# Performance work log

Measured on AMD Instinct MI355X. Metric: run time of the kernel, lower is better.

Reference implementation:

```python
import jax, jax.numpy as jnp
import numpy as np
from jax import lax

P_LEN, Q_LEN, B = 400, 60, 128
P_IN, Q_IN, H = 512, 512, 256
D = P_IN + Q_IN  # gate / GRU input size


def setup_inputs() -> dict:
    key = jax.random.key(0)
    ks = jax.random.split(key, 10)
    s = 0.05  # small init scale to keep tanh/sigmoid in sane range
    return {
        "q_input": jax.random.normal(ks[0], (Q_LEN, B, Q_IN), jnp.float32),
        "p_input": jax.random.normal(ks[1], (P_LEN, B, P_IN), jnp.float32),
        "q_mask": jnp.zeros((Q_LEN, B), dtype=bool),
        "Wq": jax.random.normal(ks[2], (2, Q_IN, H), jnp.float32) * s,
        "Wp": jax.random.normal(ks[3], (2, P_IN, H), jnp.float32) * s,
        "Ws": jax.random.normal(ks[4], (2, H, H), jnp.float32) * s,
        "v": jax.random.normal(ks[5], (2, H, 1), jnp.float32) * s,
        "gate_W": jax.random.normal(ks[6], (2, D, D), jnp.float32) * s,
        "gate_b": jnp.zeros((2, D), jnp.float32),
        "gru_Wih": jax.random.normal(ks[7], (2, 3 * H, D), jnp.float32) * s,
        "gru_Whh": jax.random.normal(ks[8], (2, 3 * H, H), jnp.float32) * s,
        "gru_bih": jnp.zeros((2, 3 * H), jnp.float32),
        "gru_bhh": jnp.zeros((2, 3 * H), jnp.float32),
    }


def _run_direction(q_input, p_input, q_mask, Wq, Wp, Ws, v,
                   gate_W, gate_b, gru_Wih, gru_Whh, gru_bih, gru_bhh,
                   reverse):
    # q_input: [Q, B, q_in], p_input: [P, B, p_in], q_mask: [Q, B] bool
    hid = Ws.shape[1]
    q_temp = jnp.einsum('qbe,eh->qbh', q_input, Wq)  # precomputed once, [Q,B,H]
    p_temp = jnp.einsum('pbe,eh->pbh', p_input, Wp)  # [P,B,H]
    mask = q_mask[:, :, None]                        # [Q,B,1]

    def step(state, xs):
        p_x, p_t = xs  # [B,p_in], [B,H]
        state_temp = state @ Ws                                   # [B,H]
        logits = jnp.tanh(q_temp + p_t[None] + state_temp[None]) @ v  # [Q,B,1]
        logits = jnp.where(mask, -jnp.inf, logits)
        weights = jax.nn.softmax(logits, axis=0)                  # over q_len
        att = jnp.sum(weights * q_input, axis=0)                  # [B,q_in]
        x = jnp.concatenate([p_x, att], axis=-1)                  # [B,D]
        x = x * jax.nn.sigmoid(x @ gate_W.T + gate_b)             # Gate
        # torch GRUCell math
        gi = x @ gru_Wih.T + gru_bih
        gh = state @ gru_Whh.T + gru_bhh
        i_r, i_z, i_n = jnp.split(gi, 3, axis=-1)
        h_r, h_z, h_n = jnp.split(gh, 3, axis=-1)
        r = jax.nn.sigmoid(i_r + h_r)
        z = jax.nn.sigmoid(i_z + h_z)
        n = jnp.tanh(i_n + r * h_n)
        new_state = (1.0 - z) * n + z * state
        return new_state, new_state

    init = jnp.zeros((p_input.shape[1], hid), p_input.dtype)
    _, out = lax.scan(step, init, (p_input, p_temp), reverse=reverse)
    return out  # [P,B,H], already in original time order (scan reverse handles it)


def reference(q_input, p_input, q_mask, Wq, Wp, Ws, v, gate_W, gate_b,
              gru_Wih, gru_Whh, gru_bih, gru_bhh):
    out_fw = _run_direction(q_input, p_input, q_mask, Wq[0], Wp[0], Ws[0], v[0],
                            gate_W[0], gate_b[0], gru_Wih[0], gru_Whh[0],
                            gru_bih[0], gru_bhh[0], reverse=False)
    out_bw = _run_direction(q_input, p_input, q_mask, Wq[1], Wp[1], Ws[1], v[1],
                            gate_W[1], gate_b[1], gru_Wih[1], gru_Whh[1],
                            gru_bih[1], gru_bhh[1], reverse=True)
    return jnp.concatenate([out_fw, out_bw], axis=-1)  # [P,B,2H]
```

## Files before the change

### kernel.cpp

```cpp
#include <hip/hip_runtime.h>

#define PL 400
#define QL 60
#define BB 128
#define EE 512
#define HH 256
#define DD 1024
#define G3 768
#define NBLK 256
#define NTHR 512
#define LDK 72

typedef __attribute__((ext_vector_type(8))) short bfrag;
typedef __attribute__((ext_vector_type(4))) float facc;
typedef __attribute__((ext_vector_type(4))) unsigned uintx4;

__device__ __forceinline__ unsigned short f2bf(float x) {
  unsigned u = __float_as_uint(x);
  return (unsigned short)((u + 0x7fffu + ((u >> 16) & 1u)) >> 16);
}
__device__ __forceinline__ float bf2f(unsigned short h) {
  return __uint_as_float(((unsigned)h) << 16);
}
__device__ __forceinline__ void split_bf(float x, unsigned short& hi, unsigned short& lo) {
  hi = f2bf(x);
  lo = f2bf(x - bf2f(hi));
}
__device__ __forceinline__ unsigned packf(float x) {
  unsigned short hi, lo;
  split_bf(x, hi, lo);
  return ((unsigned)hi << 16) | lo;
}
__device__ __forceinline__ float unpk(unsigned p) {
  return bf2f((unsigned short)(p >> 16)) + bf2f((unsigned short)(p & 0xffffu));
}
__device__ __forceinline__ float sigm(float x) {
  return __builtin_amdgcn_rcpf(1.f + __expf(-x));
}
__device__ __forceinline__ float ftanh(float x) {
  float xc = fminf(fmaxf(x, -10.f), 10.f);
  float t = __expf(2.f * xc);
  return (t - 1.f) * __builtin_amdgcn_rcpf(t + 1.f);
}

__device__ __forceinline__ float ald(const float* p) {
  return __hip_atomic_load((float*)p, __ATOMIC_RELAXED, __HIP_MEMORY_SCOPE_AGENT);
}
__device__ __forceinline__ void ast(float* p, float v) {
  __hip_atomic_store(p, v, __ATOMIC_RELAXED, __HIP_MEMORY_SCOPE_AGENT);
}
__device__ __forceinline__ unsigned aldu(const unsigned* p) {
  return __hip_atomic_load((unsigned*)p, __ATOMIC_RELAXED, __HIP_MEMORY_SCOPE_AGENT);
}
__device__ __forceinline__ void astu(unsigned* p, unsigned v) {
  __hip_atomic_store(p, v, __ATOMIC_RELAXED, __HIP_MEMORY_SCOPE_AGENT);
}
__device__ __forceinline__ unsigned long long aldull(const unsigned long long* p) {
  return __hip_atomic_load((unsigned long long*)p, __ATOMIC_RELAXED, __HIP_MEMORY_SCOPE_AGENT);
}
__device__ __forceinline__ void pollge(unsigned* f, unsigned tgt) {
  unsigned sp = 0;
  while (aldu(f) < tgt) {
    __builtin_amdgcn_s_sleep(1);
    if (++sp > (1u << 26)) break;
  }
}

constexpr size_t SZ_QT  = (size_t)2 * QL * BB * HH;
constexpr size_t SZ_PT  = (size_t)2 * PL * BB * HH;
constexpr size_t SZ_GIP = (size_t)2 * 4 * BB * G3;
constexpr size_t SZ_GHP = (size_t)2 * BB * G3;
constexpr size_t SZ_WST = (size_t)2 * HH * HH;
constexpr size_t OFF_QT  = 0;
constexpr size_t OFF_PT  = OFF_QT + SZ_QT;
constexpr size_t OFF_GIP = OFF_PT + SZ_PT;
constexpr size_t OFF_GHP = OFF_GIP + SZ_GIP;
constexpr size_t OFF_WST = OFF_GHP + SZ_GHP;
constexpr size_t F32_TOT = OFF_WST + SZ_WST;
constexpr size_t UOFF_ATTP  = 0;
constexpr size_t UOFF_XPACK = UOFF_ATTP + (size_t)2 * 2 * BB * EE;
constexpr size_t UOFF_HPACK = UOFF_XPACK + (size_t)2 * 2 * BB * DD;
constexpr size_t U_TOT      = UOFF_HPACK + (size_t)2 * BB * HH;
constexpr size_t HSZ_WQT = (size_t)2 * HH * EE;
constexpr size_t HSZ_GW  = (size_t)2 * DD * DD;
constexpr size_t HSZ_WIH = (size_t)2 * G3 * DD;
constexpr size_t HSZ_WHH = (size_t)2 * G3 * HH;
constexpr size_t HOFF_WQTH = 0;
constexpr size_t HOFF_WQTL = HOFF_WQTH + HSZ_WQT;
constexpr size_t HOFF_WPTH = HOFF_WQTL + HSZ_WQT;
constexpr size_t HOFF_WPTL = HOFF_WPTH + HSZ_WQT;
constexpr size_t HOFF_GWH  = HOFF_WPTL + HSZ_WQT;
constexpr size_t HOFF_GWL  = HOFF_GWH + HSZ_GW;
constexpr size_t HOFF_WIHH = HOFF_GWL + HSZ_GW;
constexpr size_t HOFF_WIHL = HOFF_WIHH + HSZ_WIH;
constexpr size_t HOFF_WHHH = HOFF_WIHL + HSZ_WIH;
constexpr size_t HOFF_WHHL = HOFF_WHHH + HSZ_WHH;
constexpr size_t HOFF_QIN16 = HOFF_WHHL + HSZ_WHH;
constexpr size_t H_TOT      = HOFF_QIN16 + (size_t)QL * BB * EE;

#define FA 0
#define FG 256
#define FI 320
#define FH 416
#define FC 440

__device__ __forceinline__ void gbar(unsigned* slots, unsigned gen) {
  asm volatile("" ::: "memory");
  __syncthreads();
  if (threadIdx.x == 0)
    __hip_atomic_store(&slots[blockIdx.x], gen, __ATOMIC_RELAXED, __HIP_MEMORY_SCOPE_AGENT);
  if (threadIdx.x < NBLK) pollge(&slots[threadIdx.x], gen);
  __syncthreads();
  asm volatile("" ::: "memory");
}

template <int NT, bool BSPLIT, int NCH, int ASRC>
__device__ void gemm_direct(facc* acc,
                            const unsigned short* wh, const unsigned short* wl,
                            const unsigned* apk, const float* a32, int as,
                            int kbase, int wchbase) {
  const int tid = threadIdx.x;
  const int lane = tid & 63;
  const int w = tid >> 6;
  constexpr int FN = NT / 16;
  const int lr = lane & 15;
  const int lk = (lane >> 4) << 3;
  const int row = (w << 4) + lr;

#pragma unroll 2
  for (int ch = 0; ch < NCH; ++ch) {
    const int kk = kbase + (ch << 6);
#pragma unroll
    for (int k32 = 0; k32 < 64; k32 += 32) {
      const int ko = kk + k32 + lk;
      bfrag ah, al_;
      {
        unsigned hu[4], lu[4];
        if constexpr (ASRC == 0) {
          const unsigned long long* src =
              (const unsigned long long*)(apk + (size_t)row * as + ko);
          unsigned long long d0 = aldull(src + 0);
          unsigned long long d1 = aldull(src + 1);
          unsigned long long d2 = aldull(src + 2);
          unsigned long long d3 = aldull(src + 3);
          unsigned p0 = (unsigned)d0, p1 = (unsigned)(d0 >> 32);
          unsigned p2 = (unsigned)d1, p3 = (unsigned)(d1 >> 32);
          unsigned p4 = (unsigned)d2, p5 = (unsigned)(d2 >> 32);
          unsigned p6 = (unsigned)d3, p7 = (unsigned)(d3 >> 32);
          hu[0] = (p0 >> 16) | (p1 & 0xffff0000u);  lu[0] = (p0 & 0xffffu) | (p1 << 16);
          hu[1] = (p2 >> 16) | (p3 & 0xffff0000u);  lu[1] = (p2 & 0xffffu) | (p3 << 16);
          hu[2] = (p4 >> 16) | (p5 & 0xffff0000u);  lu[2] = (p4 & 0xffffu) | (p5 << 16);
          hu[3] = (p6 >> 16) | (p7 & 0xffff0000u);  lu[3] = (p6 & 0xffffu) | (p7 << 16);
        } else {
          const float* src = a32 + (size_t)row * as + ko;
          float4 v0 = *(const float4*)src;
          float4 v1 = *(const float4*)(src + 4);
          unsigned short h0, l0, h1, l1;
          split_bf(v0.x, h0, l0); split_bf(v0.y, h1, l1);
          hu[0] = h0 | ((unsigned)h1 << 16); lu[0] = l0 | ((unsigned)l1 << 16);
          split_bf(v0.z, h0, l0); split_bf(v0.w, h1, l1);
          hu[1] = h0 | ((unsigned)h1 << 16); lu[1] = l0 | ((unsigned)l1 << 16);
          split_bf(v1.x, h0, l0); split_bf(v1.y, h1, l1);
          hu[2] = h0 | ((unsigned)h1 << 16); lu[2] = l0 | ((unsigned)l1 << 16);
          split_bf(v1.z, h0, l0); split_bf(v1.w, h1, l1);
          hu[3] = h0 | ((unsigned)h1 << 16); lu[3] = l0 | ((unsigned)l1 << 16);
        }
        uintx4 hv = {hu[0], hu[1], hu[2], hu[3]};
        uintx4 lv = {lu[0], lu[1], lu[2], lu[3]};
        ah  = __builtin_bit_cast(bfrag, hv);
        al_ = __builtin_bit_cast(bfrag, lv);
      }
      bfrag bhf[FN], blf[FN];
#pragma unroll
      for (int f = 0; f < FN; f++) {
        const int bo = ((wchbase + ch) * NT + (f << 4) + lr) * LDK + k32 + lk;
        bhf[f] = *(const bfrag*)&wh[bo];
        if constexpr (BSPLIT) blf[f] = *(const bfrag*)&wl[bo];
      }
#pragma unroll
      for (int j = 0; j < FN; j++) {
        acc[j] = __builtin_amdgcn_mfma_f32_16x16x32_bf16(al_, bhf[j], acc[j], 0, 0, 0);
        if constexpr (BSPLIT)
          acc[j] = __builtin_amdgcn_mfma_f32_16x16x32_bf16(ah, blf[j], acc[j], 0, 0, 0);
        acc[j] = __builtin_amdgcn_mfma_f32_16x16x32_bf16(ah, bhf[j], acc[j], 0, 0, 0);
      }
    }
  }
}

__device__ void gemm_pro(unsigned short* sAh, unsigned short* sAl, unsigned short* warea,
                         const float* a32,
                         const unsigned short* bh_g, const unsigned short* bl_g,
                         float* dst) {
  const int tid = threadIdx.x;
  const int lane = tid & 63;
  const int w = tid >> 6;
  const int wm = (w >> 2) << 6;
  const int wn = (w & 3) << 5;
  const int lr = lane & 15;
  const int lk = (lane >> 4) << 3;
  unsigned short* wh = warea;
  unsigned short* wl = warea + 128 * LDK;
  const facc fz = {0.f, 0.f, 0.f, 0.f};
  facc acc[4][2];
#pragma unroll
  for (int i = 0; i < 4; i++)
#pragma unroll
    for (int j = 0; j < 2; j++) acc[i][j] = fz;
  for (int ch = 0; ch < 8; ++ch) {
    const int kk0 = ch << 6;
    for (int i = tid; i < 8192; i += NTHR) {
      const int r = i >> 6, k = i & 63;
      unsigned short uh, ul;
      split_bf(a32[(size_t)r * EE + kk0 + k], uh, ul);
      sAh[r * LDK + k] = uh;
      sAl[r * LDK + k] = ul;
      wh[r * LDK + k] = bh_g[(size_t)r * EE + kk0 + k];
      wl[r * LDK + k] = bl_g[(size_t)r * EE + kk0 + k];
    }
    __syncthreads();
#pragma unroll
    for (int k32 = 0; k32 < 64; k32 += 32) {
      bfrag ah[4], al_[4], bhf[2], blf[2];
#pragma unroll
      for (int f = 0; f < 4; f++) {
        const int ao = (wm + (f << 4) + lr) * LDK + k32 + lk;
        ah[f]  = *(const bfrag*)&sAh[ao];
        al_[f] = *(const bfrag*)&sAl[ao];
      }
#pragma unroll
      for (int f = 0; f < 2; f++) {
        const int bo = (wn + (f << 4) + lr) * LDK + k32 + lk;
        bhf[f] = *(const bfrag*)&wh[bo];
        blf[f] = *(const bfrag*)&wl[bo];
      }
#pragma unroll
      for (int i = 0; i < 4; i++)
#pragma unroll
        for (int j = 0; j < 2; j++) {
          acc[i][j] = __builtin_amdgcn_mfma_f32_16x16x32_bf16(al_[i], bhf[j], acc[i][j], 0, 0, 0);
          acc[i][j] = __builtin_amdgcn_mfma_f32_16x16x32_bf16(ah[i], blf[j], acc[i][j], 0, 0, 0);
          acc[i][j] = __builtin_amdgcn_mfma_f32_16x16x32_bf16(ah[i], bhf[j], acc[i][j], 0, 0, 0);
        }
    }
    __syncthreads();
  }
  const int orow = (lane >> 4) << 2;
  const int ocol = lane & 15;
#pragma unroll
  for (int i = 0; i < 4; i++)
#pragma unroll
    for (int j = 0; j < 2; j++)
#pragma unroll
      for (int q = 0; q < 4; q++)
        dst[(size_t)(wm + (i << 4) + orow + q) * HH + (wn + (j << 4) + ocol)] = acc[i][j][q];
}

__global__ void __launch_bounds__(256) k_transpose_qp(
    const float* __restrict__ Wq, const float* __restrict__ Wp,
    unsigned short* __restrict__ wqth, unsigned short* __restrict__ wqtl,
    unsigned short* __restrict__ wpth, unsigned short* __restrict__ wptl) {
  __shared__ float tile[64 * 65];
  const int blk = blockIdx.x;
  const int mat = blk >> 6;
  const int rem = blk & 63;
  const int d = rem >> 5;
  const int rem2 = rem & 31;
  const int kt = rem2 >> 2;
  const int nt = rem2 & 3;
  const float* src = mat ? Wp : Wq;
  unsigned short* dh = mat ? wpth : wqth;
  unsigned short* dl = mat ? wptl : wqtl;
  const int tid = threadIdx.x;
  for (int i = tid; i < 4096; i += 256) {
    int kr = i >> 6, nc = i & 63;
    tile[kr * 65 + nc] = src[((size_t)d * EE + kt * 64 + kr) * HH + nt * 64 + nc];
  }
  __syncthreads();
  for (int i = tid; i < 4096; i += 256) {
    int n = i >> 6, k = i & 63;
    unsigned short hi, lo;
    split_bf(tile[k * 65 + n], hi, lo);
    size_t o = ((size_t)d * HH + nt * 64 + n) * EE + kt * 64 + k;
    dh[o] = hi; dl[o] = lo;
  }
}

__global__ void __launch_bounds__(256) k_split_w(
    const float* __restrict__ gw, const float* __restrict__ wih, const float* __restrict__ whh,
    unsigned short* __restrict__ gwh, unsigned short* __restrict__ gwl,
    unsigned short* __restrict__ wihh, unsigned short* __restrict__ wihl,
    unsigned short* __restrict__ whhh, unsigned short* __restrict__ whhl) {
  const size_t N1 = HSZ_GW, N2 = HSZ_WIH, N3 = HSZ_WHH;
  for (size_t i = (size_t)blockIdx.x * 256 + threadIdx.x; i < N1 + N2 + N3;
       i += (size_t)gridDim.x * 256) {
    float x; unsigned short *ph, *pl; size_t o;
    if (i < N1)           { o = i;           x = gw[o];  ph = gwh;  pl = gwl; }
    else if (i < N1 + N2) { o = i - N1;      x = wih[o]; ph = wihh; pl = wihl; }
    else                  { o = i - N1 - N2; x = whh[o]; ph = whhh; pl = whhl; }
    unsigned short hi, lo;
    split_bf(x, hi, lo);
    ph[o] = hi; pl[o] = lo;
  }
}

__global__ void __launch_bounds__(256) k_wst_qin(const float* __restrict__ Ws,
                                                 float* __restrict__ wst,
                                                 const float* __restrict__ qin,
                                                 unsigned short* __restrict__ qin16) {
  const size_t NQ = (size_t)QL * BB * EE;
  for (size_t i = (size_t)blockIdx.x * 256 + threadIdx.x; i < SZ_WST + NQ;
       i += (size_t)gridDim.x * 256) {
    if (i < SZ_WST) {
      int d = (int)(i >> 16);
      int j = (int)((i >> 8) & 255);
      int k = (int)(i & 255);
      wst[i] = Ws[((size_t)d * HH + k) * HH + j];
    } else {
      size_t o = i - SZ_WST;
      qin16[o] = f2bf(qin[o]);
    }
  }
}

__global__ void __launch_bounds__(NTHR, 1) pe_main(
    const float* __restrict__ qin, const float* __restrict__ pin,
    const unsigned char* __restrict__ qmask,
    const float* __restrict__ vvec, const float* __restrict__ gateb,
    const float* __restrict__ bih, const float* __restrict__ bhh,
    float* __restrict__ out,
    float* __restrict__ fws, unsigned* __restrict__ upck,
    unsigned short* __restrict__ hws, unsigned* __restrict__ bar) {
  __shared__ __align__(16) unsigned short smem[56320];
  unsigned short* sAh = smem;
  unsigned short* sAl = smem + 9216;
  unsigned short* warea = smem + 18432;
  float* fsm = (float*)smem;
  float* sv_perm   = (float*)(smem + 55296);
  float* sstv_perm = (float*)(smem + 55808);

  float* qt   = fws + OFF_QT;
  float* pt   = fws + OFF_PT;
  float* gip  = fws + OFF_GIP;
  float* ghp  = fws + OFF_GHP;
  float* wst  = fws + OFF_WST;
  unsigned* attp0 = upck + UOFF_ATTP;
  unsigned* xpck0 = upck + UOFF_XPACK;
  unsigned* hpack = upck + UOFF_HPACK;
  unsigned short* wqth = hws + HOFF_WQTH;
  unsigned short* wqtl = hws + HOFF_WQTL;
  unsigned short* wpth = hws + HOFF_WPTH;
  unsigned short* wptl = hws + HOFF_WPTL;
  unsigned short* gwh  = hws + HOFF_GWH;
  unsigned short* wihh = hws + HOFF_WIHH;
  unsigned short* wihl = hws + HOFF_WIHL;
  unsigned short* whhh = hws + HOFF_WHHH;
  unsigned short* whhl = hws + HOFF_WHHL;
  const unsigned short* qin16 = hws + HOFF_QIN16;
  unsigned* flg = bar + 256;

  const int blk = blockIdx.x;
  const int tid = threadIdx.x;
  const int lane = tid & 63;
  const int w = tid >> 6;

  const bool isGate = (blk < 64);
  const bool isGi   = (blk >= 64 && blk < 160);
  const bool isGh   = (blk >= 160 && blk < 184);
  const int gd = blk >> 5, gct = blk & 31, coloff = gct * 32;
  const int gi_g = blk - 64, id_ = gi_g / 48, ir = gi_g % 48;
  const int int_ = ir >> 2, iks = ir & 3;
  const int gh_g = blk - 160, hd = gh_g / 12, hnt = gh_g % 12;

  for (int tt = blk; tt < 1840; tt += NBLK) {
    if (tt < 1600) {
      int d = tt / 800, rem = tt % 800, mt = rem >> 1, ntp = rem & 1;
      gemm_pro(sAh, sAl, warea, pin + (size_t)mt * BB * EE,
               wpth + ((size_t)d * HH + ntp * 128) * EE,
               wptl + ((size_t)d * HH + ntp * 128) * EE,
               pt + ((size_t)d * PL * BB + (size_t)mt * BB) * HH + ntp * 128);
    } else {
      int u2 = tt - 1600;
      int d = u2 / 120, rem = u2 % 120, mt = rem >> 1, ntp = rem & 1;
      gemm_pro(sAh, sAl, warea, qin + (size_t)mt * BB * EE,
               wqth + ((size_t)d * HH + ntp * 128) * EE,
               wqtl + ((size_t)d * HH + ntp * 128) * EE,
               qt + ((size_t)d * QL * BB + (size_t)mt * BB) * HH + ntp * 128);
    }
  }

  if (isGate) {
    const unsigned short* src = gwh + (size_t)(gd * DD + coloff) * DD;
    for (int i = tid; i < 32768; i += NTHR) {
      int ch = i >> 11, n = (i >> 6) & 31, k = i & 63;
      warea[(ch * 32 + n) * LDK + k] = src[(size_t)n * DD + ch * 64 + k];
    }
  } else if (isGi) {
    const unsigned short* sh = wihh + (size_t)(id_ * G3 + int_ * 64) * DD + iks * 256;
    const unsigned short* sl = wihl + (size_t)(id_ * G3 + int_ * 64) * DD + iks * 256;
    for (int i = tid; i < 16384; i += NTHR) {
      int ch = i >> 12, n = (i >> 6) & 63, k = i & 63;
      warea[(ch * 64 + n) * LDK + k]         = sh[(size_t)n * DD + ch * 64 + k];
      warea[18432 + (ch * 64 + n) * LDK + k] = sl[(size_t)n * DD + ch * 64 + k];
    }
  } else if (isGh) {
    const unsigned short* sh = whhh + (size_t)(hd * G3 + hnt * 64) * HH;
    const unsigned short* sl = whhl + (size_t)(hd * G3 + hnt * 64) * HH;
    for (int i = tid; i < 16384; i += NTHR) {
      int ch = i >> 12, n = (i >> 6) & 63, k = i & 63;
      warea[(ch * 64 + n) * LDK + k]         = sh[(size_t)n * HH + ch * 64 + k];
      warea[18432 + (ch * 64 + n) * LDK + k] = sl[(size_t)n * HH + ch * 64 + k];
    }
  }

  __builtin_amdgcn_fence(__ATOMIC_RELEASE, "agent");
  gbar(bar, 1);

  const int d_ab = blk >> 7, b_ab = blk & 127;
  if (tid < 256) {
    sv_perm[tid] = vvec[d_ab * HH + tid];
    sstv_perm[tid] = 0.f;
  }
  const bool qmv = (tid < 64 && lane < QL) ? (qmask[lane * BB + b_ab] != 0) : false;
  __syncthreads();

  facc pinacc[2];
  if (isGate) {
    const facc fz = {0.f, 0.f, 0.f, 0.f};
    pinacc[0] = fz; pinacc[1] = fz;
    const int t0 = gd ? (PL - 1) : 0;
    gemm_direct<32, false, 8, 1>(pinacc, warea, nullptr,
                                 nullptr, pin + (size_t)t0 * BB * EE, EE, 0, 0);
  }

  float hreg = 0.f;
  float* sm = fsm;
  float* slog = fsm + 512;
  float* swgt = fsm + 576;
  float* spart = fsm + 896;
  float* hrow = fsm + 1408;

  for (int s = 0; s < PL; ++s) {
    const int par = s & 1;
    unsigned* attp = attp0 + (size_t)par * 2 * BB * EE;
    unsigned* xpack = xpck0 + (size_t)par * 2 * BB * DD;
    const unsigned gen = (unsigned)(s + 1);

    {
      const int d = d_ab, b = b_ab;
      const int t = d ? (PL - 1 - s) : s;
      if (tid < 256) {
        float ptv = __builtin_nontemporal_load(&pt[(((size_t)d * PL + t) * BB + b) * HH + tid]);
        sm[tid] = sstv_perm[tid] + ptv;
      }
      __syncthreads();
      for (int q = w; q < QL; q += 8) {
        float a = 0.f;
#pragma unroll
        for (int jj = 0; jj < 4; jj++) {
          int j = lane + jj * 64;
          a += ftanh(qt[(((size_t)d * QL + q) * BB + b) * HH + j] + sm[j]) * sv_perm[j];
        }
        for (int off = 32; off; off >>= 1) a += __shfl_down(a, off, 64);
        if (lane == 0) slog[q] = a;
      }
      __syncthreads();
      if (tid < 64) {
        float x = -3.0e38f;
        if (lane < QL) {
          x = slog[lane];
          if (qmv) x = -3.0e38f;
        }
        float mx = x;
        for (int off = 32; off; off >>= 1) mx = fmaxf(mx, __shfl_xor(mx, off, 64));
        float e = (lane < QL) ? __expf(x - mx) : 0.f;
        float sum2 = e;
        for (int off = 32; off; off >>= 1) sum2 += __shfl_xor(sum2, off, 64);
        if (lane < QL) swgt[lane] = e * __builtin_amdgcn_rcpf(sum2);
      }
      __syncthreads();
      {
        const int c = tid;
        float a0 = 0.f, a1 = 0.f, a2 = 0.f, a3 = 0.f;
        const unsigned short* qb = qin16 + (size_t)b * EE + c;
        for (int q = 0; q < QL; q += 4) {
          a0 += swgt[q]     * bf2f(qb[(size_t)q * BB * EE]);
          a1 += swgt[q + 1] * bf2f(qb[(size_t)(q + 1) * BB * EE]);
          a2 += swgt[q + 2] * bf2f(qb[(size_t)(q + 2) * BB * EE]);
          a3 += swgt[q + 3] * bf2f(qb[(size_t)(q + 3) * BB * EE]);
        }
        astu(&attp[((size_t)d * BB + b) * EE + c], packf((a0 + a1) + (a2 + a3)));
      }
      __syncthreads();
      if (tid == 0) astu(&flg[FA + d_ab * 128 + b_ab], gen);
    }

    const int orow = (lane >> 4) << 2;
    const int ocol = lane & 15;
    const int rbase = w << 4;

    if (isGate) {
      if (tid < 128) pollge(&flg[FA + gd * 128 + tid], gen);
      __syncthreads();
      gemm_direct<32, false, 8, 0>(pinacc, warea, nullptr,
                                   attp + (size_t)gd * BB * EE, nullptr, EE, 0, 8);
      {
        const int t = gd ? (PL - 1 - s) : s;
        const float* pin_t = pin + (size_t)t * BB * EE;
#pragma unroll
        for (int i = 0; i < 2; i++)
#pragma unroll
          for (int q = 0; q < 4; q++) {
            const int row = rbase + orow + q;
            const int gcol = coloff + (i << 4) + ocol;
            float uv = (gct < 16) ? pin_t[(size_t)row * EE + gcol]
                                  : unpk(aldu(&attp[((size_t)gd * BB + row) * EE + gcol - EE]));
            float x = uv * sigm(pinacc[i][q] + gateb[(size_t)gd * DD + gcol]);
            astu(&xpack[((size_t)gd * BB + row) * DD + gcol], packf(x));
          }
      }
      __syncthreads();
      if (tid == 0) astu(&flg[FG + gd * 32 + gct], gen);
      if (s + 1 < PL) {
        const facc fz = {0.f, 0.f, 0.f, 0.f};
        pinacc[0] = fz; pinacc[1] = fz;
        const int t2 = gd ? (PL - 2 - s) : (s + 1);
        gemm_direct<32, false, 8, 1>(pinacc, warea, nullptr,
                                     nullptr, pin + (size_t)t2 * BB * EE, EE, 0, 0);
      }
    } else if (isGi) {
      if (tid < 8) pollge(&flg[FG + id_ * 32 + iks * 8 + tid], gen);
      __syncthreads();
      const facc fz = {0.f, 0.f, 0.f, 0.f};
      facc acc[4] = {fz, fz, fz, fz};
      gemm_direct<64, true, 4, 0>(acc, warea, warea + 18432,
                                  xpack + (size_t)id_ * BB * DD, nullptr, DD, iks * 256, 0);
#pragma unroll
      for (int j = 0; j < 4; j++)
#pragma unroll
        for (int q = 0; q < 4; q++) {
          const int row = rbase + orow + q;
          const int col = int_ * 64 + (j << 4) + ocol;
          ast(&gip[((size_t)(id_ * 4 + iks) * BB + row) * G3 + col], acc[j][q]);
        }
      __syncthreads();
      if (tid == 0) astu(&flg[FI + id_ * 48 + ir], gen);
    } else if (isGh) {
      if (s > 0 && tid < 128) pollge(&flg[FC + hd * 128 + tid], (unsigned)s);
      __syncthreads();
      const facc fz = {0.f, 0.f, 0.f, 0.f};
      facc acc[4] = {fz, fz, fz, fz};
      gemm_direct<64, true, 4, 0>(acc, warea, warea + 18432,
                                  hpack + (size_t)hd * BB * HH, nullptr, HH, 0, 0);
#pragma unroll
      for (int j = 0; j < 4; j++)
#pragma unroll
        for (int q = 0; q < 4; q++) {
          const int row = rbase + orow + q;
          const int col = hnt * 64 + (j << 4) + ocol;
          ast(&ghp[((size_t)hd * BB + row) * G3 + col], acc[j][q]);
        }
      __syncthreads();
      if (tid == 0) astu(&flg[FH + hd * 12 + hnt], gen);
    }

    {
      if (tid < 48) pollge(&flg[FI + d_ab * 48 + tid], gen);
      else if (tid < 60) pollge(&flg[FH + d_ab * 12 + (tid - 48)], gen);
      __syncthreads();
      const int d = d_ab, b = b_ab;
      const int j = tid & 255, half = tid >> 8;
      const int t = d ? (PL - 1 - s) : s;
      const size_t rb = (size_t)d * BB + b;
      float gi3[3], gh3[3];
#pragma unroll
      for (int c3 = 0; c3 < 3; c3++) {
        float acc2 = bih[(size_t)d * G3 + c3 * HH + j];
#pragma unroll
        for (int ks = 0; ks < 4; ks++)
          acc2 += ald(&gip[((size_t)(d * 4 + ks) * BB + b) * G3 + c3 * HH + j]);
        gi3[c3] = acc2;
        gh3[c3] = ald(&ghp[rb * G3 + c3 * HH + j]) + bhh[(size_t)d * G3 + c3 * HH + j];
      }
      float r = sigm(gi3[0] + gh3[0]);
      float z = sigm(gi3[1] + gh3[1]);
      float n = ftanh(gi3[2] + r * gh3[2]);
      float hn = (1.f - z) * n + z * hreg;
      hreg = hn;
      if (half == 0) {
        __builtin_nontemporal_store(hn, &out[((size_t)t * BB + b) * 512 + d * HH + j]);
        astu(&hpack[rb * HH + j], packf(hn));
        hrow[j] = hn;
      }
      __syncthreads();
      if (tid == 0) astu(&flg[FC + d_ab * 128 + b_ab], gen);
      float part = 0.f;
      const float* wr = wst + ((size_t)d * HH + j) * HH + (half << 7);
      const float* hr = hrow + (half << 7);
#pragma unroll
      for (int k = 0; k < 128; k += 4) {
        float4 w4 = *(const float4*)&wr[k];
        float4 h4 = *(const float4*)&hr[k];
        part += w4.x * h4.x + w4.y * h4.y + w4.z * h4.z + w4.w * h4.w;
      }
      spart[tid] = part;
      __syncthreads();
      if (tid < 256) sstv_perm[tid] = spart[tid] + spart[tid + 256];
      __syncthreads();
    }
  }
}

extern "C" void kernel_launch(void* const* d_in, const int* in_sizes, int n_in,
                              void* d_out, int out_size, void* d_ws, size_t ws_size,
                              hipStream_t stream) {
  const float* qin = (const float*)d_in[0];
  const float* pin = (const float*)d_in[1];
  const unsigned char* qmask = (const unsigned char*)d_in[2];
  const float* Wq  = (const float*)d_in[3];
  const float* Wp  = (const float*)d_in[4];
  const float* Ws  = (const float*)d_in[5];
  const float* v   = (const float*)d_in[6];
  const float* gw  = (const float*)d_in[7];
  const float* gb  = (const float*)d_in[8];
  const float* wih = (const float*)d_in[9];
  const float* whh = (const float*)d_in[10];
  const float* bih = (const float*)d_in[11];
  const float* bhh = (const float*)d_in[12];
  float* out = (float*)d_out;

  char* base = (char*)d_ws;
  float* fws = (float*)base;
  unsigned* upck = (unsigned*)(base + F32_TOT * sizeof(float));
  unsigned short* hws = (unsigned short*)(base + F32_TOT * sizeof(float) + U_TOT * sizeof(unsigned));
  unsigned* bar = (unsigned*)(base + F32_TOT * sizeof(float) + U_TOT * sizeof(unsigned) +
                              H_TOT * sizeof(unsigned short));
  size_t need = F32_TOT * sizeof(float) + U_TOT * sizeof(unsigned) +
                H_TOT * sizeof(unsigned short) + 8192;
  if (ws_size < need) return;

  hipMemsetAsync(upck + UOFF_HPACK, 0, (size_t)2 * BB * HH * sizeof(unsigned), stream);
  hipMemsetAsync(bar, 0, 4096, stream);

  k_transpose_qp<<<128, 256, 0, stream>>>(Wq, Wp,
      hws + HOFF_WQTH, hws + HOFF_WQTL, hws + HOFF_WPTH, hws + HOFF_WPTL);
  k_split_w<<<1024, 256, 0, stream>>>(gw, wih, whh,
      hws + HOFF_GWH, hws + HOFF_GWL, hws + HOFF_WIHH, hws + HOFF_WIHL,
      hws + HOFF_WHHH, hws + HOFF_WHHL);
  k_wst_qin<<<2048, 256, 0, stream>>>(Ws, fws + OFF_WST, qin,
                                      hws + HOFF_QIN16);
  pe_main<<<NBLK, NTHR, 0, stream>>>(qin, pin, qmask, v, gb, bih, bhh, out,
                                     fws, upck, hws, bar);
}
```

Baseline: 20.54 ms.

## Move q/p projection GEMMs to separate kernel and add release fences on flags

The Wq/Wp projection GEMMs move out of the persistent pe_main loop into a standalone k_qtpt kernel launched with 1840 blocks. Kernel-launch ordering now replaces the grid-wide barrier that pe_main used to need before its recurrent phase. Each flag publish gets an agent-scope release fence, each poll gets a compiler scheduling fence, and the output store becomes a normal store instead of a nontemporal one. This lets the GEMM phase use full-device occupancy rather than 256 persistent blocks, at the cost of an extra launch and extra fence instructions on every recurrent step.

```diff
diff --git a/kernel.cpp b/kernel.cpp
--- a/kernel.cpp
+++ b/kernel.cpp
@@ -64,6 +64,10 @@
     __builtin_amdgcn_s_sleep(1);
     if (++sp > (1u << 26)) break;
   }
+}
+__device__ __forceinline__ void poll_fence() {
+  __builtin_amdgcn_sched_barrier(0);
+  asm volatile("" ::: "memory");
 }
 
 constexpr size_t SZ_QT  = (size_t)2 * QL * BB * HH;
@@ -103,16 +107,6 @@
 #define FI 320
 #define FH 416
 #define FC 440
-
-__device__ __forceinline__ void gbar(unsigned* slots, unsigned gen) {
-  asm volatile("" ::: "memory");
-  __syncthreads();
-  if (threadIdx.x == 0)
-    __hip_atomic_store(&slots[blockIdx.x], gen, __ATOMIC_RELAXED, __HIP_MEMORY_SCOPE_AGENT);
-  if (threadIdx.x < NBLK) pollge(&slots[threadIdx.x], gen);
-  __syncthreads();
-  asm volatile("" ::: "memory");
-}
 
 template <int NT, bool BSPLIT, int NCH, int ASRC>
 __device__ void gemm_direct(facc* acc,
@@ -323,6 +317,32 @@
   }
 }
 
+__global__ void __launch_bounds__(NTHR) k_qtpt(
+    const float* __restrict__ qin, const float* __restrict__ pin,
+    const unsigned short* __restrict__ wqth, const unsigned short* __restrict__ wqtl,
+    const unsigned short* __restrict__ wpth, const unsigned short* __restrict__ wptl,
+    float* __restrict__ qt, float* __restrict__ pt) {
+  __shared__ __align__(16) unsigned short smem[55296];
+  unsigned short* sAh = smem;
+  unsigned short* sAl = smem + 9216;
+  unsigned short* warea = smem + 18432;
+  const int tt = blockIdx.x;
+  if (tt < 1600) {
+    int d = tt / 800, rem = tt % 800, mt = rem >> 1, ntp = rem & 1;
+    gemm_pro(sAh, sAl, warea, pin + (size_t)mt * BB * EE,
+             wpth + ((size_t)d * HH + ntp * 128) * EE,
+             wptl + ((size_t)d * HH + ntp * 128) * EE,
+             pt + ((size_t)d * PL * BB + (size_t)mt * BB) * HH + ntp * 128);
+  } else {
+    int u2 = tt - 1600;
+    int d = u2 / 120, rem = u2 % 120, mt = rem >> 1, ntp = rem & 1;
+    gemm_pro(sAh, sAl, warea, qin + (size_t)mt * BB * EE,
+             wqth + ((size_t)d * HH + ntp * 128) * EE,
+             wqtl + ((size_t)d * HH + ntp * 128) * EE,
+             qt + ((size_t)d * QL * BB + (size_t)mt * BB) * HH + ntp * 128);
+  }
+}
+
 __global__ void __launch_bounds__(NTHR, 1) pe_main(
     const float* __restrict__ qin, const float* __restrict__ pin,
     const unsigned char* __restrict__ qmask,
@@ -332,25 +352,19 @@
     float* __restrict__ fws, unsigned* __restrict__ upck,
     unsigned short* __restrict__ hws, unsigned* __restrict__ bar) {
   __shared__ __align__(16) unsigned short smem[56320];
-  unsigned short* sAh = smem;
-  unsigned short* sAl = smem + 9216;
   unsigned short* warea = smem + 18432;
   float* fsm = (float*)smem;
   float* sv_perm   = (float*)(smem + 55296);
   float* sstv_perm = (float*)(smem + 55808);
 
-  float* qt   = fws + OFF_QT;
-  float* pt   = fws + OFF_PT;
+  const float* qt = fws + OFF_QT;
+  const float* pt = fws + OFF_PT;
   float* gip  = fws + OFF_GIP;
   float* ghp  = fws + OFF_GHP;
-  float* wst  = fws + OFF_WST;
+  const float* wst = fws + OFF_WST;
   unsigned* attp0 = upck + UOFF_ATTP;
   unsigned* xpck0 = upck + UOFF_XPACK;
   unsigned* hpack = upck + UOFF_HPACK;
-  unsigned short* wqth = hws + HOFF_WQTH;
-  unsigned short* wqtl = hws + HOFF_WQTL;
-  unsigned short* wpth = hws + HOFF_WPTH;
-  unsigned short* wptl = hws + HOFF_WPTL;
   unsigned short* gwh  = hws + HOFF_GWH;
   unsigned short* wihh = hws + HOFF_WIHH;
   unsigned short* wihl = hws + HOFF_WIHL;
@@ -372,23 +386,6 @@
   const int int_ = ir >> 2, iks = ir & 3;
   const int gh_g = blk - 160, hd = gh_g / 12, hnt = gh_g % 12;
 
-  for (int tt = blk; tt < 1840; tt += NBLK) {
-    if (tt < 1600) {
-      int d = tt / 800, rem = tt % 800, mt = rem >> 1, ntp = rem & 1;
-      gemm_pro(sAh, sAl, warea, pin + (size_t)mt * BB * EE,
-               wpth + ((size_t)d * HH + ntp * 128) * EE,
-               wptl + ((size_t)d * HH + ntp * 128) * EE,
-               pt + ((size_t)d * PL * BB + (size_t)mt * BB) * HH + ntp * 128);
-    } else {
-      int u2 = tt - 1600;
-      int d = u2 / 120, rem = u2 % 120, mt = rem >> 1, ntp = rem & 1;
-      gemm_pro(sAh, sAl, warea, qin + (size_t)mt * BB * EE,
-               wqth + ((size_t)d * HH + ntp * 128) * EE,
-               wqtl + ((size_t)d * HH + ntp * 128) * EE,
-               qt + ((size_t)d * QL * BB + (size_t)mt * BB) * HH + ntp * 128);
-    }
-  }
-
   if (isGate) {
     const unsigned short* src = gwh + (size_t)(gd * DD + coloff) * DD;
     for (int i = tid; i < 32768; i += NTHR) {
@@ -412,9 +409,6 @@
       warea[18432 + (ch * 64 + n) * LDK + k] = sl[(size_t)n * HH + ch * 64 + k];
     }
   }
-
-  __builtin_amdgcn_fence(__ATOMIC_RELEASE, "agent");
-  gbar(bar, 1);
 
   const int d_ab = blk >> 7, b_ab = blk & 127;
   if (tid < 256) {
@@ -492,7 +486,10 @@
         astu(&attp[((size_t)d * BB + b) * EE + c], packf((a0 + a1) + (a2 + a3)));
       }
       __syncthreads();
-      if (tid == 0) astu(&flg[FA + d_ab * 128 + b_ab], gen);
+      if (tid == 0) {
+        __builtin_amdgcn_fence(__ATOMIC_RELEASE, "agent");
+        astu(&flg[FA + d_ab * 128 + b_ab], gen);
+      }
     }
 
     const int orow = (lane >> 4) << 2;
@@ -502,6 +499,7 @@
     if (isGate) {
       if (tid < 128) pollge(&flg[FA + gd * 128 + tid], gen);
       __syncthreads();
+      poll_fence();
       gemm_direct<32, false, 8, 0>(pinacc, warea, nullptr,
                                    attp + (size_t)gd * BB * EE, nullptr, EE, 0, 8);
       {
@@ -520,7 +518,10 @@
           }
       }
       __syncthreads();
-      if (tid == 0) astu(&flg[FG + gd * 32 + gct], gen);
+      if (tid == 0) {
+        __builtin_amdgcn_fence(__ATOMIC_RELEASE, "agent");
+        astu(&flg[FG + gd * 32 + gct], gen);
+      }
       if (s + 1 < PL) {
         const facc fz = {0.f, 0.f, 0.f, 0.f};
         pinacc[0] = fz; pinacc[1] = fz;
@@ -531,6 +532,7 @@
     } else if (isGi) {
       if (tid < 8) pollge(&flg[FG + id_ * 32 + iks * 8 + tid], gen);
       __syncthreads();
+      poll_fence();
       const facc fz = {0.f, 0.f, 0.f, 0.f};
       facc acc[4] = {fz, fz, fz, fz};
       gemm_direct<64, true, 4, 0>(acc, warea, warea + 18432,
@@ -544,10 +546,14 @@
           ast(&gip[((size_t)(id_ * 4 + iks) * BB + row) * G3 + col], acc[j][q]);
         }
       __syncthreads();
-      if (tid == 0) astu(&flg[FI + id_ * 48 + ir], gen);
+      if (tid == 0) {
+        __builtin_amdgcn_fence(__ATOMIC_RELEASE, "agent");
+        astu(&flg[FI + id_ * 48 + ir], gen);
+      }
     } else if (isGh) {
       if (s > 0 && tid < 128) pollge(&flg[FC + hd * 128 + tid], (unsigned)s);
       __syncthreads();
+      poll_fence();
       const facc fz = {0.f, 0.f, 0.f, 0.f};
       facc acc[4] = {fz, fz, fz, fz};
       gemm_direct<64, true, 4, 0>(acc, warea, warea + 18432,
@@ -561,13 +567,17 @@
           ast(&ghp[((size_t)hd * BB + row) * G3 + col], acc[j][q]);
         }
       __syncthreads();
-      if (tid == 0) astu(&flg[FH + hd * 12 + hnt], gen);
+      if (tid == 0) {
+        __builtin_amdgcn_fence(__ATOMIC_RELEASE, "agent");
+        astu(&flg[FH + hd * 12 + hnt], gen);
+      }
     }
 
     {
       if (tid < 48) pollge(&flg[FI + d_ab * 48 + tid], gen);
       else if (tid < 60) pollge(&flg[FH + d_ab * 12 + (tid - 48)], gen);
       __syncthreads();
+      poll_fence();
       const int d = d_ab, b = b_ab;
       const int j = tid & 255, half = tid >> 8;
       const int t = d ? (PL - 1 - s) : s;
@@ -588,12 +598,15 @@
       float hn = (1.f - z) * n + z * hreg;
       hreg = hn;
       if (half == 0) {
-        __builtin_nontemporal_store(hn, &out[((size_t)t * BB + b) * 512 + d * HH + j]);
+        out[((size_t)t * BB + b) * 512 + d * HH + j] = hn;
         astu(&hpack[rb * HH + j], packf(hn));
         hrow[j] = hn;
       }
       __syncthreads();
-      if (tid == 0) astu(&flg[FC + d_ab * 128 + b_ab], gen);
+      if (tid == 0) {
+        __builtin_amdgcn_fence(__ATOMIC_RELEASE, "agent");
+        astu(&flg[FC + d_ab * 128 + b_ab], gen);
+      }
       float part = 0.f;
       const float* wr = wst + ((size_t)d * HH + j) * HH + (half << 7);
       const float* hr = hrow + (half << 7);
@@ -649,6 +662,9 @@
       hws + HOFF_WHHH, hws + HOFF_WHHL);
   k_wst_qin<<<2048, 256, 0, stream>>>(Ws, fws + OFF_WST, qin,
                                       hws + HOFF_QIN16);
+  k_qtpt<<<1840, NTHR, 0, stream>>>(qin, pin,
+      hws + HOFF_WQTH, hws + HOFF_WQTL, hws + HOFF_WPTH, hws + HOFF_WPTL,
+      fws + OFF_QT, fws + OFF_PT);
   pe_main<<<NBLK, NTHR, 0, stream>>>(qin, pin, qmask, v, gb, bih, bhh, out,
                                      fws, upck, hws, bar);
 }
```

Measured after the change: 24.32 ms (median of 2 runs). 1.18x slower.
